# Kernel tuning notes

Measured on AMD Instinct MI355X. Metric: run time of the kernel, lower is better.

## Reference

```python
import math
import jax, jax.numpy as jnp
import numpy as np

B, S, D, H = 2, 2048, 2048, 16
HD = D // H  # 128
EPS = 1e-5


def setup_inputs() -> dict:
    key = jax.random.key(0)
    ks = jax.random.split(key, 7)
    x = jax.random.normal(ks[0], (B, S, D), jnp.float32)
    # RoPE tables: (seqlen, head_dim//2)
    theta = 10000.0
    inv_freq = 1.0 / (theta ** (np.arange(0, HD, 2, dtype=np.float32) / HD))
    t = np.arange(S, dtype=np.float32)
    freqs = np.outer(t, inv_freq)  # (S, HD//2)
    freqs_cos = jnp.asarray(np.cos(freqs), jnp.float32)
    freqs_sin = jnp.asarray(np.sin(freqs), jnp.float32)
    sc = 0.02
    wq = jax.random.normal(ks[1], (D, D), jnp.float32) * sc  # stored (in, out)
    wk = jax.random.normal(ks[2], (D, D), jnp.float32) * sc
    wv = jax.random.normal(ks[3], (D, D), jnp.float32) * sc
    wu = jax.random.normal(ks[4], (D, D), jnp.float32) * sc
    wo = jax.random.normal(ks[5], (D, D), jnp.float32) * sc
    norm_w = jnp.ones((D,), jnp.float32)
    return {"x": x, "freqs_cos": freqs_cos, "freqs_sin": freqs_sin,
            "wq": wq, "wk": wk, "wv": wv, "wu": wu, "wo": wo, "norm_w": norm_w}


def _rope(t, cos, sin):
    # t: (B, S, H, HD); cos/sin: (S, HD//2)
    tr = t.reshape(t.shape[:-1] + (-1, 2))
    r, i = tr[..., 0], tr[..., 1]
    c = cos[None, :, None, :]
    s = sin[None, :, None, :]
    out_r = r * c - i * s
    out_i = r * s + i * c
    return jnp.stack([out_r, out_i], axis=-1).reshape(t.shape)


def reference(x, freqs_cos, freqs_sin, wq, wk, wv, wu, wo, norm_w):
    b, s, d = x.shape
    h = jax.nn.silu(x)  # pre-projection SiLU on the input
    q = (h @ wq).reshape(b, s, H, HD)
    k = (h @ wk).reshape(b, s, H, HD)
    v = (h @ wv).reshape(b, s, H, HD)
    u = h @ wu  # reshape->transpose->flatten in original is identity on (b,s,d)
    q = _rope(q, freqs_cos, freqs_sin)
    k = _rope(k, freqs_cos, freqs_sin)
    # scores: (b, H, s, s)
    scores = jnp.einsum('bqhd,bkhd->bhqk', q, k) / math.sqrt(HD)
    causal = jnp.tril(jnp.ones((s, s), bool))  # mask!=0 positions zeroed; silu(0)=0
    scores = jnp.where(causal[None, None], jax.nn.silu(scores), 0.0)
    out = jnp.einsum('bhqk,bkhd->bqhd', scores, v).reshape(b, s, d)
    # RMSNorm
    out = out * jax.lax.rsqrt(jnp.mean(out * out, axis=-1, keepdims=True) + EPS)
    out = out * norm_w
    out = out * u
    return out @ wo
```

## Files before the change

kernel.cpp:

```cpp
#include <hip/hip_runtime.h>
#include <hip/hip_bf16.h>
#include <cstdint>

typedef __attribute__((ext_vector_type(8))) short bf16x8;
typedef __attribute__((ext_vector_type(4))) float f32x4;
typedef unsigned short u16;

constexpr int B = 2, S = 2048, D = 2048, H = 16, HD = 128;
constexpr int M = B * S;
constexpr int NQKU = 6144;
constexpr int ATT_LD = 3072;
constexpr float SCALE = 0.08838834764831845f;

static __device__ __forceinline__ float b2f(u16 u) {
    union { float f; uint32_t i; } v; v.i = ((uint32_t)u) << 16; return v.f;
}
static __device__ __forceinline__ u16 f2b(float f) {
    union { float f; uint32_t i; } v; v.f = f;
    uint32_t x = v.i;
    return (u16)((x + 0x7FFFu + ((x >> 16) & 1u)) >> 16);
}

__device__ __forceinline__ void gll16(const void* g, void* l) {
    __builtin_amdgcn_global_load_lds(
        (const __attribute__((address_space(1))) uint32_t*)g,
        (__attribute__((address_space(3))) uint32_t*)l, 16, 0, 0);
}

#define BAR() do { asm volatile("" ::: "memory"); __builtin_amdgcn_s_barrier(); \
                   asm volatile("" ::: "memory"); } while (0)

__global__ __launch_bounds__(256) void silu_cast(const float* __restrict__ x,
                                                 u16* __restrict__ h, int n) {
    int i = (blockIdx.x * 256 + threadIdx.x) * 4;
    if (i >= n) return;
    float4 v = *(const float4*)(x + i);
    ushort4 o;
    o.x = f2b(v.x / (1.f + __expf(-v.x)));
    o.y = f2b(v.y / (1.f + __expf(-v.y)));
    o.z = f2b(v.z / (1.f + __expf(-v.z)));
    o.w = f2b(v.w / (1.f + __expf(-v.w)));
    *(ushort4*)(h + i) = o;
}

__global__ __launch_bounds__(256) void wcast(const float* __restrict__ w,
                                             u16* __restrict__ wT) {
    __shared__ float t[64][65];
    int tx = threadIdx.x & 63, ty = threadIdx.x >> 6;
    int kb = blockIdx.y * 64, nb = blockIdx.x * 64;
    for (int r = ty; r < 64; r += 4)
        t[r][tx] = w[(size_t)(kb + r) * D + nb + tx];
    __syncthreads();
    for (int r = ty; r < 64; r += 4)
        wT[(size_t)(nb + r) * D + kb + tx] = f2b(t[tx][r]);
}

__global__ __launch_bounds__(512, 2)
void gemm_qkuv(const u16* __restrict__ A, const u16* __restrict__ BT,
               u16* __restrict__ qku, u16* __restrict__ vt) {
    __shared__ u16 lds[65536];
    const int tid = threadIdx.x;
    const int lane = tid & 63, wid = tid >> 6;
    const int wm = wid >> 2, wn = wid & 3;
    const int l16 = lane & 15, lq = lane >> 4;

    const int orig = blockIdx.x;
    const int swz = (orig & 7) * 64 + (orig >> 3);
    const int mt = swz & 15, nt = swz >> 4;
    const int m0 = mt * 256, n0 = nt * 256;

    const int srow = tid >> 2;
    const int ce = ((tid & 3) * 8) ^ (((tid >> 5) & 1) << 4);
    const int rdx = (lq * 16) ^ (((l16 >> 3) & 1) << 5);

    const u16* As0 = A + (size_t)(m0 + srow) * D + ce;
    const u16* Bs0 = BT + (size_t)(n0 + srow) * D + ce;

    {
        u16* dA = lds + wid * 512;
        u16* dB = lds + 16384 + wid * 512;
        gll16(As0,                    dA);
        gll16(As0 + (size_t)128 * D,  dA + 8192);
        gll16(Bs0,                    dB);
        gll16(Bs0 + (size_t)128 * D,  dB + 8192);
        gll16(As0 + 32,                    dA + 4096);
        gll16(As0 + 32 + (size_t)128 * D,  dA + 8192 + 4096);
        gll16(Bs0 + 32,                    dB + 4096);
        gll16(Bs0 + 32 + (size_t)128 * D,  dB + 8192 + 4096);
    }
    asm volatile("s_waitcnt vmcnt(4)" ::: "memory");
    BAR();

    f32x4 acc[8][4] = {};
    bf16x8 a[8];
    const int rbB = (wn & 1) * 4096;

#define LOAD_A(kk)                                                            \
    _Pragma("unroll") for (int mi = 0; mi < 8; ++mi)                          \
        a[mi] = *(const bf16x8*)(Abase + (kk) * 8192 +                        \
                                 (mi * 16 + l16) * 64 + rdx);
#define LOAD_B(dst, nia, kk)                                                  \
    dst = *(const bf16x8*)(Bbase + (kk) * 8192 + rbB +                        \
                           ((nia) * 16 + l16) * 64 + rdx);
#define MFMA2(n0i, n1i)                                                       \
    __builtin_amdgcn_s_setprio(1);                                            \
    _Pragma("unroll") for (int mi = 0; mi < 8; ++mi) {                        \
        acc[mi][n0i] = __builtin_amdgcn_mfma_f32_16x16x32_bf16(a[mi], b0,     \
                            acc[mi][n0i], 0, 0, 0);                           \
        acc[mi][n1i] = __builtin_amdgcn_mfma_f32_16x16x32_bf16(a[mi], b1,     \
                            acc[mi][n1i], 0, 0, 0);                           \
    }                                                                          \
    __builtin_amdgcn_s_setprio(0);

    for (int kt = 0; kt < 32; ++kt) {
        const int buf = kt & 1;
        const char* Abase = (const char*)lds + buf * 65536 + wm * 16384;
        const char* Bbase = (const char*)lds + 32768 + buf * 65536 + (wn >> 1) * 16384;
        const bool st = (kt + 1) < 32;
        const u16* Asrc = As0 + (kt + 1) * 64;
        const u16* Bsrc = Bs0 + (kt + 1) * 64;
        u16* dA = lds + (buf ^ 1) * 32768 + wid * 512;
        u16* dB = dA + 16384;
        bf16x8 b0, b1;

        LOAD_A(0);
        LOAD_B(b0, 0, 0);
        LOAD_B(b1, 1, 0);
        if (st) { gll16(Asrc, dA); gll16(Asrc + (size_t)128 * D, dA + 8192); }
        BAR();
        MFMA2(0, 1);
        BAR();
        LOAD_B(b0, 2, 0);
        LOAD_B(b1, 3, 0);
        if (st) { gll16(Bsrc, dB); gll16(Bsrc + (size_t)128 * D, dB + 8192); }
        BAR();
        MFMA2(2, 3);
        if (kt == 31) asm volatile("s_waitcnt vmcnt(0)" ::: "memory");
        else         asm volatile("s_waitcnt vmcnt(4)" ::: "memory");
        BAR();
        LOAD_A(1);
        LOAD_B(b0, 0, 1);
        LOAD_B(b1, 1, 1);
        if (st) { gll16(Asrc + 32, dA + 4096); gll16(Asrc + 32 + (size_t)128 * D, dA + 8192 + 4096); }
        BAR();
        MFMA2(0, 1);
        BAR();
        LOAD_B(b0, 2, 1);
        LOAD_B(b1, 3, 1);
        if (st) { gll16(Bsrc + 32, dB + 4096); gll16(Bsrc + 32 + (size_t)128 * D, dB + 8192 + 4096); }
        BAR();
        MFMA2(2, 3);
        if (kt < 31) asm volatile("s_waitcnt vmcnt(4)" ::: "memory");
        BAR();
    }
#undef LOAD_A
#undef LOAD_B
#undef MFMA2

    if (n0 >= NQKU) {
#pragma unroll
        for (int mi = 0; mi < 8; ++mi)
#pragma unroll
            for (int ni = 0; ni < 4; ++ni) {
                int c = n0 - NQKU + wn * 64 + ni * 16 + l16;
                int hh = c >> 7, d = c & 127;
                int row0 = m0 + wm * 128 + mi * 16 + lq * 4;
                int bb = row0 >> 11, s0 = row0 & 2047;
                ushort4 pk = make_ushort4(f2b(acc[mi][ni][0]), f2b(acc[mi][ni][1]),
                                          f2b(acc[mi][ni][2]), f2b(acc[mi][ni][3]));
                *(ushort4*)(vt + (((size_t)(bb * H + hh) * HD + d) * S + s0)) = pk;
            }
    } else {
#pragma unroll
        for (int mi = 0; mi < 8; ++mi)
#pragma unroll
            for (int ni = 0; ni < 4; ++ni)
#pragma unroll
                for (int r = 0; r < 4; ++r) {
                    int row = m0 + wm * 128 + mi * 16 + lq * 4 + r;
                    int col = n0 + wn * 64 + ni * 16 + l16;
                    qku[(size_t)row * NQKU + col] = f2b(acc[mi][ni][r]);
                }
    }
}

__global__ __launch_bounds__(256)
void gemm_bt_f32(const u16* __restrict__ A, const u16* __restrict__ BT,
                 float* __restrict__ out, int lda, int ldc, int Kk) {
    __shared__ u16 As[128 * 32];
    __shared__ u16 Bs[128 * 32];
    const int tid = threadIdx.x;
    const int lane = tid & 63, w = tid >> 6;
    const int wm = w >> 1, wn = w & 1;
    const int l16 = lane & 15, lq = lane >> 4;
    const int m0 = blockIdx.y * 128, n0 = blockIdx.x * 128;
    const int rs = lane >> 2;
    const int cs = (lane & 3) * 8;
    f32x4 acc[4][4] = {};

    const u16* Ab = A + (size_t)(m0 + w * 32 + rs) * lda + cs;
    const u16* Bb = BT + (size_t)(n0 + w * 32 + rs) * Kk + cs;
    u16* Al = As + w * 32 * 32;
    u16* Bl = Bs + w * 32 * 32;

    for (int k0 = 0; k0 < Kk; k0 += 32) {
        gll16(Ab + k0, Al);
        gll16(Ab + k0 + (size_t)16 * lda, Al + 16 * 32);
        gll16(Bb + k0, Bl);
        gll16(Bb + k0 + (size_t)16 * Kk, Bl + 16 * 32);
        __syncthreads();
        bf16x8 af[4], bfr[4];
#pragma unroll
        for (int mi = 0; mi < 4; mi++)
            af[mi] = *(const bf16x8*)(As + (wm * 64 + mi * 16 + l16) * 32 + lq * 8);
#pragma unroll
        for (int ni = 0; ni < 4; ni++)
            bfr[ni] = *(const bf16x8*)(Bs + (wn * 64 + ni * 16 + l16) * 32 + lq * 8);
#pragma unroll
        for (int mi = 0; mi < 4; mi++)
#pragma unroll
            for (int ni = 0; ni < 4; ni++)
                acc[mi][ni] = __builtin_amdgcn_mfma_f32_16x16x32_bf16(
                    af[mi], bfr[ni], acc[mi][ni], 0, 0, 0);
        __syncthreads();
    }
#pragma unroll
    for (int mi = 0; mi < 4; mi++)
#pragma unroll
        for (int ni = 0; ni < 4; ni++)
#pragma unroll
            for (int r = 0; r < 4; r++) {
                int row = m0 + wm * 64 + mi * 16 + lq * 4 + r;
                int col = n0 + wn * 64 + ni * 16 + l16;
                out[(size_t)row * ldc + col] = acc[mi][ni][r];
            }
}

__global__ __launch_bounds__(256)
void reformat(const u16* __restrict__ qku, const float* __restrict__ fc,
              const float* __restrict__ fs, u16* __restrict__ qr,
              u16* __restrict__ kr) {
    int bh = blockIdx.x;
    int s0 = blockIdx.y * 64;
    int b = bh >> 4, h = bh & 15;
    int tid = threadIdx.x;
#pragma unroll
    for (int i = 0; i < 16; ++i) {
        int p = tid + i * 256;
        int row = p >> 6, pp = p & 63;
        int sgl = s0 + row;
        float c = fc[sgl * 64 + pp], sn = fs[sgl * 64 + pp];
        size_t src = (size_t)(b * S + sgl) * NQKU + h * HD + 2 * pp;
        size_t dst = ((size_t)bh * S + sgl) * HD + 2 * pp;
        {
            uint32_t qv = *(const uint32_t*)(qku + src);
            float r = b2f((u16)(qv & 0xffff)), im = b2f((u16)(qv >> 16));
            uint32_t o = (uint32_t)f2b(r * c - im * sn) |
                         ((uint32_t)f2b(r * sn + im * c) << 16);
            *(uint32_t*)(qr + dst) = o;
        }
        {
            uint32_t kv = *(const uint32_t*)(qku + src + 2048);
            float r = b2f((u16)(kv & 0xffff)), im = b2f((u16)(kv >> 16));
            uint32_t o = (uint32_t)f2b(r * c - im * sn) |
                         ((uint32_t)f2b(r * sn + im * c) << 16);
            *(uint32_t*)(kr + dst) = o;
        }
    }
}

__global__ __launch_bounds__(256)
void hstu_attn(const u16* __restrict__ qr, const u16* __restrict__ kr,
               const u16* __restrict__ vt, float* __restrict__ att) {
    const int bh = blockIdx.y, slot = blockIdx.x;
    const int b = bh >> 4, h = bh & 15;
    const int tid = threadIdx.x, lane = tid & 63, w = tid >> 6;
    const int l16 = lane & 15, lq = lane >> 4;
    const int wm = w >> 1, wn = w & 1;
    constexpr int LDK = 136, LDV = 72, LDS_ = 72;
    __shared__ u16 k_l[64 * LDK];
    __shared__ u16 v_l[128 * LDV];
    __shared__ u16 s_l[64 * LDS_];

    for (int pass = 0; pass < 2; ++pass) {
        const int t = pass ? (31 - slot) : slot;
        const int q0 = t * 64;
        bf16x8 qf[2][4];
#pragma unroll
        for (int mi = 0; mi < 2; mi++)
#pragma unroll
            for (int kk = 0; kk < 4; kk++)
                qf[mi][kk] = *(const bf16x8*)(qr +
                    ((size_t)bh * S + q0 + wm * 32 + mi * 16 + l16) * HD + kk * 32 + lq * 8);
        f32x4 acco[2][4] = {};

        for (int kt = 0; kt <= t; ++kt) {
            const int k0 = kt * 64;
            __syncthreads();
#pragma unroll
            for (int i = 0; i < 4; ++i) {
                int u = tid + i * 256;
                int row = u >> 4, cb = (u & 15) * 8;
                *(int4*)(k_l + row * LDK + cb) =
                    *(const int4*)(kr + ((size_t)bh * S + k0 + row) * HD + cb);
            }
#pragma unroll
            for (int i = 0; i < 4; ++i) {
                int u = tid + i * 256;
                int row = u >> 3, cb = (u & 7) * 8;
                *(int4*)(v_l + row * LDV + cb) =
                    *(const int4*)(vt + ((size_t)bh * HD + row) * S + k0 + cb);
            }
            __syncthreads();
            f32x4 accs[2][2] = {};
            bf16x8 kf[2][4];
#pragma unroll
            for (int ni = 0; ni < 2; ni++)
#pragma unroll
                for (int kk = 0; kk < 4; kk++)
                    kf[ni][kk] = *(const bf16x8*)(k_l + (wn * 32 + ni * 16 + l16) * LDK +
                                                  kk * 32 + lq * 8);
#pragma unroll
            for (int kk = 0; kk < 4; kk++)
#pragma unroll
                for (int mi = 0; mi < 2; mi++)
#pragma unroll
                    for (int ni = 0; ni < 2; ni++)
                        accs[mi][ni] = __builtin_amdgcn_mfma_f32_16x16x32_bf16(
                            qf[mi][kk], kf[ni][kk], accs[mi][ni], 0, 0, 0);
            const bool dg = (kt == t);
#pragma unroll
            for (int mi = 0; mi < 2; mi++)
#pragma unroll
                for (int ni = 0; ni < 2; ni++)
#pragma unroll
                    for (int r = 0; r < 4; r++) {
                        int qrow = wm * 32 + mi * 16 + lq * 4 + r;
                        int krow = wn * 32 + ni * 16 + l16;
                        float vv = accs[mi][ni][r] * SCALE;
                        vv = (!dg || krow <= qrow) ? vv / (1.f + __expf(-vv)) : 0.f;
                        s_l[qrow * LDS_ + krow] = f2b(vv);
                    }
            __syncthreads();
#pragma unroll
            for (int kk = 0; kk < 2; kk++) {
                bf16x8 vf[4];
#pragma unroll
                for (int ni = 0; ni < 4; ni++)
                    vf[ni] = *(const bf16x8*)(v_l + (wn * 64 + ni * 16 + l16) * LDV +
                                              kk * 32 + lq * 8);
#pragma unroll
                for (int mi = 0; mi < 2; mi++) {
                    bf16x8 sf = *(const bf16x8*)(s_l + (wm * 32 + mi * 16 + l16) * LDS_ +
                                                 kk * 32 + lq * 8);
#pragma unroll
                    for (int ni = 0; ni < 4; ni++)
                        acco[mi][ni] = __builtin_amdgcn_mfma_f32_16x16x32_bf16(
                            sf, vf[ni], acco[mi][ni], 0, 0, 0);
                }
            }
        }
#pragma unroll
        for (int mi = 0; mi < 2; mi++)
#pragma unroll
            for (int ni = 0; ni < 4; ni++)
#pragma unroll
                for (int r = 0; r < 4; r++) {
                    int qrow = q0 + wm * 32 + mi * 16 + lq * 4 + r;
                    int d = wn * 64 + ni * 16 + l16;
                    att[(size_t)(b * S + qrow) * ATT_LD + h * HD + d] = acco[mi][ni][r];
                }
    }
}

__global__ __launch_bounds__(256)
void rms_mul(const float* __restrict__ att, u16* __restrict__ qku,
             const float* __restrict__ nw) {
    int row = blockIdx.x;
    int tid = threadIdx.x;
    const float* a = att + (size_t)row * ATT_LD + tid * 8;
    float4 v0 = *(const float4*)(a);
    float4 v1 = *(const float4*)(a + 4);
    float ss = v0.x * v0.x + v0.y * v0.y + v0.z * v0.z + v0.w * v0.w +
               v1.x * v1.x + v1.y * v1.y + v1.z * v1.z + v1.w * v1.w;
#pragma unroll
    for (int off = 32; off > 0; off >>= 1) ss += __shfl_down(ss, off, 64);
    __shared__ float red[4];
    int lane = tid & 63, w = tid >> 6;
    if (lane == 0) red[w] = ss;
    __syncthreads();
    float rs = rsqrtf((red[0] + red[1] + red[2] + red[3]) * (1.f / D) + 1e-5f);
    int col = tid * 8;
    u16* up = qku + (size_t)row * NQKU + 4096 + col;
    u16 ut[8];
    *(int4*)ut = *(const int4*)up;
    float f[8] = {v0.x, v0.y, v0.z, v0.w, v1.x, v1.y, v1.z, v1.w};
    u16 o[8];
#pragma unroll
    for (int j = 0; j < 8; j++)
        o[j] = f2b(f[j] * rs * nw[col + j] * b2f(ut[j]));
    *(int4*)up = *(int4*)o;
}

extern "C" void kernel_launch(void* const* d_in, const int* in_sizes, int n_in,
                              void* d_out, int out_size, void* d_ws, size_t ws_size,
                              hipStream_t stream) {
    const float* x  = (const float*)d_in[0];
    const float* fc = (const float*)d_in[1];
    const float* fs = (const float*)d_in[2];
    const float* wq = (const float*)d_in[3];
    const float* wk = (const float*)d_in[4];
    const float* wv = (const float*)d_in[5];
    const float* wu = (const float*)d_in[6];
    const float* wo = (const float*)d_in[7];
    const float* nw = (const float*)d_in[8];
    float* out = (float*)d_out;

    char* ws = (char*)d_ws;
    const size_t WSZ = (size_t)D * D * sizeof(u16);
    u16* h_b  = (u16*)(ws);
    u16* wT   = (u16*)(ws + 2 * WSZ);
    u16* qku  = (u16*)(ws + 7 * WSZ);
    u16* vt   = (u16*)(ws + 13 * WSZ);
    u16* k_r  = (u16*)(ws + 15 * WSZ);
    u16* q_r  = h_b;
    float* att = (float*)qku;

    silu_cast<<<M * D / 1024, 256, 0, stream>>>(x, h_b, M * D);
    dim3 wg(32, 32);
    wcast<<<wg, 256, 0, stream>>>(wq, wT + 0 * (size_t)D * D);
    wcast<<<wg, 256, 0, stream>>>(wk, wT + 1 * (size_t)D * D);
    wcast<<<wg, 256, 0, stream>>>(wu, wT + 2 * (size_t)D * D);
    wcast<<<wg, 256, 0, stream>>>(wv, wT + 3 * (size_t)D * D);
    wcast<<<wg, 256, 0, stream>>>(wo, wT + 4 * (size_t)D * D);

    gemm_qkuv<<<512, 512, 0, stream>>>(h_b, wT, qku, vt);

    reformat<<<dim3(32, 32), 256, 0, stream>>>(qku, fc, fs, q_r, k_r);
    hstu_attn<<<dim3(16, 32), 256, 0, stream>>>(q_r, k_r, vt, att);
    rms_mul<<<M, 256, 0, stream>>>(att, qku, nw);
    gemm_bt_f32<<<dim3(D / 128, M / 128), 256, 0, stream>>>(
        qku + 4096, wT + 4 * (size_t)D * D, out, NQKU, D, D);
}
```

Baseline: 366.3 us.

## Restructure HSTU attention into 128-row tiles with async LDS prefetch and swizzle

The attention kernel moves from 64x64 tiles with 4 waves per block to 128x128 tiles with 8 waves, where each wave owns 16 query rows and keeps its own score slab in shared memory. K and V tiles are now loaded with direct global-to-LDS loads into XOR-swizzled layouts. The next K tile is prefetched during the PV phase and the next V tile after it, with setprio around the MFMA sections. The aim is to cut LDS bank conflicts, hide global load latency, and reduce barriers per key tile. In exchange the grid shrinks to 256 blocks, the causal tiles are coarser, and the hand-written vmcnt waits are fragile.

Result: no change. 361.7 us (-1.3%).

```diff
diff --git a/kernel.cpp b/kernel.cpp
--- a/kernel.cpp
+++ b/kernel.cpp
@@ -269,108 +269,118 @@
     }
 }
 
-__global__ __launch_bounds__(256)
+__global__ __launch_bounds__(512, 2)
 void hstu_attn(const u16* __restrict__ qr, const u16* __restrict__ kr,
                const u16* __restrict__ vt, float* __restrict__ att) {
-    const int bh = blockIdx.y, slot = blockIdx.x;
+    __shared__ u16 k_l[16384];
+    __shared__ u16 v_l[16384];
+    __shared__ u16 s_l[8 * 16 * 136];
+    const int bh = blockIdx.x & 31, slot = blockIdx.x >> 5;
     const int b = bh >> 4, h = bh & 15;
     const int tid = threadIdx.x, lane = tid & 63, w = tid >> 6;
     const int l16 = lane & 15, lq = lane >> 4;
-    const int wm = w >> 1, wn = w & 1;
-    constexpr int LDK = 136, LDV = 72, LDS_ = 72;
-    __shared__ u16 k_l[64 * LDK];
-    __shared__ u16 v_l[128 * LDV];
-    __shared__ u16 s_l[64 * LDS_];
+    u16* s_w = s_l + w * 16 * 136;
+
+    const u16* kb = kr + (size_t)bh * S * HD;
+    const u16* vb = vt + (size_t)bh * HD * S;
+
+    const int irow0 = tid >> 4, iu0 = tid & 15;
+
+#define STAGE_K(k0_)                                                          \
+    _Pragma("unroll") for (int r_ = 0; r_ < 4; ++r_) {                        \
+        int row_ = irow0 + r_ * 32;                                           \
+        int uc_ = iu0 ^ (row_ & 7);                                           \
+        gll16(kb + (size_t)(k0_ + row_) * HD + uc_ * 8,                       \
+              k_l + ((w * 64 + r_ * 512) << 3));                              \
+    }
+#define STAGE_V(k0_)                                                          \
+    _Pragma("unroll") for (int r_ = 0; r_ < 4; ++r_) {                        \
+        int row_ = irow0 + r_ * 32;                                           \
+        int uc_ = iu0 ^ (row_ & 7);                                           \
+        gll16(vb + (size_t)row_ * S + (k0_) + uc_ * 8,                        \
+              v_l + ((w * 64 + r_ * 512) << 3));                              \
+    }
 
     for (int pass = 0; pass < 2; ++pass) {
-        const int t = pass ? (31 - slot) : slot;
-        const int q0 = t * 64;
-        bf16x8 qf[2][4];
-#pragma unroll
-        for (int mi = 0; mi < 2; mi++)
-#pragma unroll
-            for (int kk = 0; kk < 4; kk++)
-                qf[mi][kk] = *(const bf16x8*)(qr +
-                    ((size_t)bh * S + q0 + wm * 32 + mi * 16 + l16) * HD + kk * 32 + lq * 8);
-        f32x4 acco[2][4] = {};
+        const int t = pass ? (15 - slot) : slot;
+        const int q0 = t * 128;
+        const int qg0 = q0 + w * 16;
+
+        bf16x8 qf[4];
+#pragma unroll
+        for (int kk = 0; kk < 4; ++kk)
+            qf[kk] = *(const bf16x8*)(qr + ((size_t)bh * S + qg0 + l16) * HD +
+                                      kk * 32 + lq * 8);
+        f32x4 acco[8] = {};
+
+        STAGE_K(0);
+        STAGE_V(0);
+        asm volatile("s_waitcnt vmcnt(0)" ::: "memory");
+        BAR();
 
         for (int kt = 0; kt <= t; ++kt) {
-            const int k0 = kt * 64;
-            __syncthreads();
-#pragma unroll
-            for (int i = 0; i < 4; ++i) {
-                int u = tid + i * 256;
-                int row = u >> 4, cb = (u & 15) * 8;
-                *(int4*)(k_l + row * LDK + cb) =
-                    *(const int4*)(kr + ((size_t)bh * S + k0 + row) * HD + cb);
-            }
-#pragma unroll
-            for (int i = 0; i < 4; ++i) {
-                int u = tid + i * 256;
-                int row = u >> 3, cb = (u & 7) * 8;
-                *(int4*)(v_l + row * LDV + cb) =
-                    *(const int4*)(vt + ((size_t)bh * HD + row) * S + k0 + cb);
-            }
-            __syncthreads();
-            f32x4 accs[2][2] = {};
-            bf16x8 kf[2][4];
-#pragma unroll
-            for (int ni = 0; ni < 2; ni++)
-#pragma unroll
-                for (int kk = 0; kk < 4; kk++)
-                    kf[ni][kk] = *(const bf16x8*)(k_l + (wn * 32 + ni * 16 + l16) * LDK +
-                                                  kk * 32 + lq * 8);
-#pragma unroll
-            for (int kk = 0; kk < 4; kk++)
-#pragma unroll
-                for (int mi = 0; mi < 2; mi++)
-#pragma unroll
-                    for (int ni = 0; ni < 2; ni++)
-                        accs[mi][ni] = __builtin_amdgcn_mfma_f32_16x16x32_bf16(
-                            qf[mi][kk], kf[ni][kk], accs[mi][ni], 0, 0, 0);
+            const int k0 = kt * 128;
+            const bool st = kt < t;
+            f32x4 accs[8] = {};
+            __builtin_amdgcn_s_setprio(1);
+#pragma unroll
+            for (int kk = 0; kk < 4; ++kk)
+#pragma unroll
+                for (int ni = 0; ni < 8; ++ni) {
+                    int row = ni * 16 + l16;
+                    bf16x8 kf = *(const bf16x8*)(k_l + row * 128 +
+                                ((kk * 32 + lq * 8) ^ ((row & 7) << 3)));
+                    accs[ni] = __builtin_amdgcn_mfma_f32_16x16x32_bf16(
+                        qf[kk], kf, accs[ni], 0, 0, 0);
+                }
+            __builtin_amdgcn_s_setprio(0);
             const bool dg = (kt == t);
 #pragma unroll
-            for (int mi = 0; mi < 2; mi++)
-#pragma unroll
-                for (int ni = 0; ni < 2; ni++)
-#pragma unroll
-                    for (int r = 0; r < 4; r++) {
-                        int qrow = wm * 32 + mi * 16 + lq * 4 + r;
-                        int krow = wn * 32 + ni * 16 + l16;
-                        float vv = accs[mi][ni][r] * SCALE;
-                        vv = (!dg || krow <= qrow) ? vv / (1.f + __expf(-vv)) : 0.f;
-                        s_l[qrow * LDS_ + krow] = f2b(vv);
-                    }
-            __syncthreads();
-#pragma unroll
-            for (int kk = 0; kk < 2; kk++) {
-                bf16x8 vf[4];
-#pragma unroll
-                for (int ni = 0; ni < 4; ni++)
-                    vf[ni] = *(const bf16x8*)(v_l + (wn * 64 + ni * 16 + l16) * LDV +
-                                              kk * 32 + lq * 8);
-#pragma unroll
-                for (int mi = 0; mi < 2; mi++) {
-                    bf16x8 sf = *(const bf16x8*)(s_l + (wm * 32 + mi * 16 + l16) * LDS_ +
-                                                 kk * 32 + lq * 8);
-#pragma unroll
-                    for (int ni = 0; ni < 4; ni++)
-                        acco[mi][ni] = __builtin_amdgcn_mfma_f32_16x16x32_bf16(
-                            sf, vf[ni], acco[mi][ni], 0, 0, 0);
+            for (int ni = 0; ni < 8; ++ni)
+#pragma unroll
+                for (int r = 0; r < 4; ++r) {
+                    int qrow = lq * 4 + r;
+                    int krow = ni * 16 + l16;
+                    float vv = accs[ni][r] * SCALE;
+                    vv = (!dg || (k0 + krow <= qg0 + qrow))
+                             ? vv / (1.f + __expf(-vv)) : 0.f;
+                    s_w[qrow * 136 + krow] = f2b(vv);
+                }
+            BAR();
+            if (st) STAGE_K(k0 + 128);
+            if (st) asm volatile("s_waitcnt vmcnt(4)" ::: "memory");
+            else    asm volatile("s_waitcnt vmcnt(0)" ::: "memory");
+            BAR();
+            __builtin_amdgcn_s_setprio(1);
+#pragma unroll
+            for (int kk = 0; kk < 4; ++kk) {
+                bf16x8 sf = *(const bf16x8*)(s_w + l16 * 136 + kk * 32 + lq * 8);
+#pragma unroll
+                for (int ni = 0; ni < 8; ++ni) {
+                    int row = ni * 16 + l16;
+                    bf16x8 vf = *(const bf16x8*)(v_l + row * 128 +
+                                ((kk * 32 + lq * 8) ^ ((row & 7) << 3)));
+                    acco[ni] = __builtin_amdgcn_mfma_f32_16x16x32_bf16(
+                        sf, vf, acco[ni], 0, 0, 0);
                 }
             }
+            __builtin_amdgcn_s_setprio(0);
+            BAR();
+            if (st) {
+                STAGE_V(k0 + 128);
+                asm volatile("s_waitcnt vmcnt(4)" ::: "memory");
+            }
+            BAR();
         }
 #pragma unroll
-        for (int mi = 0; mi < 2; mi++)
-#pragma unroll
-            for (int ni = 0; ni < 4; ni++)
-#pragma unroll
-                for (int r = 0; r < 4; r++) {
-                    int qrow = q0 + wm * 32 + mi * 16 + lq * 4 + r;
-                    int d = wn * 64 + ni * 16 + l16;
-                    att[(size_t)(b * S + qrow) * ATT_LD + h * HD + d] = acco[mi][ni][r];
-                }
-    }
+        for (int ni = 0; ni < 8; ++ni)
+#pragma unroll
+            for (int r = 0; r < 4; ++r)
+                att[(size_t)(b * S + qg0 + lq * 4 + r) * ATT_LD +
+                    h * HD + ni * 16 + l16] = acco[ni][r];
+    }
+#undef STAGE_K
+#undef STAGE_V
 }
 
 __global__ __launch_bounds__(256)
@@ -437,7 +447,7 @@
     gemm_qkuv<<<512, 512, 0, stream>>>(h_b, wT, qku, vt);
 
     reformat<<<dim3(32, 32), 256, 0, stream>>>(qku, fc, fs, q_r, k_r);
-    hstu_attn<<<dim3(16, 32), 256, 0, stream>>>(q_r, k_r, vt, att);
+    hstu_attn<<<256, 512, 0, stream>>>(q_r, k_r, vt, att);
     rms_mul<<<M, 256, 0, stream>>>(att, qku, nw);
     gemm_bt_f32<<<dim3(D / 128, M / 128), 256, 0, stream>>>(
         qku + 4096, wT + 4 * (size_t)D * D, out, NQKU, D, D);
```
